# Kernel optimization log

Measured on AMD Instinct MI355X. Metric: run time of the kernel, lower is better.

## Reference

```python
import jax, jax.numpy as jnp
import numpy as np

N = 50000          # nodes
E = 1600000        # edges
F_IN = 128         # node_features
H = 256            # hidden_dim
A = 16             # action_dim
G = 64             # num graphs in batch


def _sage_conv(x, src, dst, Wl, bl, Wr, num_nodes):
    # PyG SAGEConv (aggr='mean'): out = lin_l(mean_{j in N(i)} x_j) + lin_r(x_i)
    msgs = x[src]                                              # [E, F] gather
    agg = jax.ops.segment_sum(msgs, dst, num_segments=num_nodes)
    cnt = jax.ops.segment_sum(jnp.ones((src.shape[0], 1), x.dtype), dst,
                              num_segments=num_nodes)
    mean = agg / jnp.maximum(cnt, 1.0)                         # [N, F]
    return mean @ Wl + bl + x @ Wr


def setup_inputs() -> dict:
    key = jax.random.key(0)
    ks = jax.random.split(key, 16)
    s = lambda k, sh: jax.random.normal(k, sh, dtype=jnp.float32) * (1.0 / np.sqrt(sh[0]))
    inp = {
        "x": jax.random.normal(ks[0], (N, F_IN), dtype=jnp.float32),
        "edge_index": jax.random.randint(ks[1], (2, E), 0, N, dtype=jnp.int32),
        "batch": jnp.sort(jax.random.randint(ks[2], (N,), 0, G, dtype=jnp.int32)),
        # SAGEConv 1
        "Wl1": s(ks[3], (F_IN, H)), "bl1": jnp.zeros((H,), jnp.float32), "Wr1": s(ks[4], (F_IN, H)),
        # SAGEConv 2
        "Wl2": s(ks[5], (H, H)), "bl2": jnp.zeros((H,), jnp.float32), "Wr2": s(ks[6], (H, H)),
        # actor MLP
        "Wa1": s(ks[7], (H, H)), "ba1": jnp.zeros((H,), jnp.float32),
        "Wa2": s(ks[8], (H, A)), "ba2": jnp.zeros((A,), jnp.float32),
        # critic MLP
        "Wc1": s(ks[9], (H, H)), "bc1": jnp.zeros((H,), jnp.float32),
        "Wc2": s(ks[10], (H, 1)), "bc2": jnp.zeros((1,), jnp.float32),
    }
    return inp


def reference(x, edge_index, batch, Wl1, bl1, Wr1, Wl2, bl2, Wr2,
              Wa1, ba1, Wa2, ba2, Wc1, bc1, Wc2, bc2):
    src, dst = edge_index[0], edge_index[1]
    h = jax.nn.relu(_sage_conv(x, src, dst, Wl1, bl1, Wr1, N))
    h = jax.nn.relu(_sage_conv(h, src, dst, Wl2, bl2, Wr2, N))
    # global_mean_pool over graph ids
    pooled = jax.ops.segment_sum(h, batch, num_segments=G)
    gcnt = jax.ops.segment_sum(jnp.ones((N, 1), h.dtype), batch, num_segments=G)
    g = pooled / jnp.maximum(gcnt, 1.0)                        # [G, H]
    mu = jax.nn.relu(g @ Wa1 + ba1) @ Wa2 + ba2                # [G, A]
    value = jax.nn.relu(g @ Wc1 + bc1) @ Wc2 + bc2             # [G, 1]
    return mu, value
```

## Files before the change

kernel.cpp:

```cpp
#include <hip/hip_runtime.h>
#include <hip/hip_bf16.h>
#include <hip/hip_fp8.h>

#define NN 50000
#define NE 1600000
#define FIN 128
#define HH 256
#define GG 64
#define AA 16
#define NRANGE 4
#define RSZ (NN / NRANGE)
#define CAP 128
#define NFB ((NE / 4 + 255) / 256 * NRANGE)

typedef __attribute__((ext_vector_type(8))) short short8;
typedef __attribute__((ext_vector_type(4))) float f32x4;
typedef __attribute__((ext_vector_type(4))) int   i32x4;
typedef __attribute__((ext_vector_type(4))) uint  u32x4;

static __device__ __forceinline__ ushort f2b(float f) {
    union { __hip_bfloat16 h; ushort u; } v; v.h = __float2bfloat16(f); return v.u;
}
static __device__ __forceinline__ float b2f_lo(uint a) {
    union { float f; uint u; } v; v.u = a << 16; return v.f;
}
template<int SEL>
static __device__ __forceinline__ float f8tof(uint u) {
#if __has_builtin(__builtin_amdgcn_cvt_f32_fp8)
    return __builtin_amdgcn_cvt_f32_fp8(u, SEL);
#else
    union { unsigned char c; __hip_fp8_e4m3 f; } v;
    v.c = (u >> (SEL * 8)) & 0xFF;
    return (float)v.f;
#endif
}
static __device__ __forceinline__ unsigned char ftof8(float f) {
    __hip_fp8_e4m3 v(f);
    return *reinterpret_cast<unsigned char*>(&v);
}

__global__ void k_prep(const int* __restrict__ src, const int* __restrict__ dst,
                       int* __restrict__ cnt, ushort* __restrict__ csr16,
                       const float* __restrict__ x, ushort* __restrict__ xb,
                       unsigned char* __restrict__ xf8,
                       const float* __restrict__ Wl1, const float* __restrict__ Wr1,
                       ushort* __restrict__ Wt1,
                       const float* __restrict__ Wl2, const float* __restrict__ Wr2,
                       ushort* __restrict__ Wt2) {
    int b = blockIdx.x, t = threadIdx.x;
    if (b < NFB) {
        int range = b & (NRANGE - 1);
        int i = (b / NRANGE) * 256 + t;
        if (i >= NE / 4) return;
        i32x4 d = __builtin_nontemporal_load(reinterpret_cast<const i32x4*>(dst) + i);
        i32x4 s = __builtin_nontemporal_load(reinterpret_cast<const i32x4*>(src) + i);
        int lo = range * RSZ, hi = lo + RSZ;
        if (d.x >= lo && d.x < hi) {
            int sl = atomicAdd(&cnt[d.x], 1);
            if (sl < CAP) csr16[(size_t)d.x * CAP + sl] = (ushort)s.x;
        }
        if (d.y >= lo && d.y < hi) {
            int sl = atomicAdd(&cnt[d.y], 1);
            if (sl < CAP) csr16[(size_t)d.y * CAP + sl] = (ushort)s.y;
        }
        if (d.z >= lo && d.z < hi) {
            int sl = atomicAdd(&cnt[d.z], 1);
            if (sl < CAP) csr16[(size_t)d.z * CAP + sl] = (ushort)s.z;
        }
        if (d.w >= lo && d.w < hi) {
            int sl = atomicAdd(&cnt[d.w], 1);
            if (sl < CAP) csr16[(size_t)d.w * CAP + sl] = (ushort)s.w;
        }
    } else if (b < NFB + 6250) {
        int i = (b - NFB) * 256 + t;
        float4 v = reinterpret_cast<const float4*>(x)[i];
        ushort4 o; o.x = f2b(v.x); o.y = f2b(v.y); o.z = f2b(v.z); o.w = f2b(v.w);
        reinterpret_cast<ushort4*>(xb)[i] = o;
        uchar4 p; p.x = ftof8(v.x); p.y = ftof8(v.y); p.z = ftof8(v.z); p.w = ftof8(v.w);
        reinterpret_cast<uchar4*>(xf8)[i] = p;
    } else if (b < NFB + 6506) {
        int i = (b - NFB - 6250) * 256 + t;
        int n = i / 256, k = i % 256;
        float v = (k < 128) ? Wl1[k * HH + n] : Wr1[(k - 128) * HH + n];
        Wt1[i] = f2b(v);
    } else {
        int i = (b - NFB - 6506) * 256 + t;
        int n = i / 512, k = i % 512;
        float v = (k < 256) ? Wl2[k * HH + n] : Wr2[(k - 256) * HH + n];
        Wt2[i] = f2b(v);
    }
}

template<int C>
__global__ void __launch_bounds__(256) k_gatherf8(
        const int* __restrict__ cnt, const ushort* __restrict__ csr16,
        const unsigned char* __restrict__ feat, ushort* __restrict__ agg) {
    constexpr int V = C / 64;
    int wid = threadIdx.x >> 6, lane = threadIdx.x & 63;
    int node = blockIdx.x * 4 + wid;
    if (node >= NN) return;
    int deg = cnt[node]; if (deg > CAP) deg = CAP;
    const ushort* row = csr16 + (size_t)node * CAP;
    const unsigned char* fp = feat + lane * V;
    float acc[V];
#pragma unroll
    for (int i = 0; i < V; i++) acc[i] = 0.0f;

    int t = 0;
    for (; t + 3 < deg; t += 4) {
        int s0 = __builtin_nontemporal_load(row + t);
        int s1 = __builtin_nontemporal_load(row + t + 1);
        int s2 = __builtin_nontemporal_load(row + t + 2);
        int s3 = __builtin_nontemporal_load(row + t + 3);
        if constexpr (V == 2) {
            uint u0 = *(const ushort*)(fp + (size_t)s0 * C);
            uint u1 = *(const ushort*)(fp + (size_t)s1 * C);
            uint u2 = *(const ushort*)(fp + (size_t)s2 * C);
            uint u3 = *(const ushort*)(fp + (size_t)s3 * C);
            acc[0] += (f8tof<0>(u0) + f8tof<0>(u1)) + (f8tof<0>(u2) + f8tof<0>(u3));
            acc[1] += (f8tof<1>(u0) + f8tof<1>(u1)) + (f8tof<1>(u2) + f8tof<1>(u3));
        } else {
            uint u0 = *(const uint*)(fp + (size_t)s0 * C);
            uint u1 = *(const uint*)(fp + (size_t)s1 * C);
            uint u2 = *(const uint*)(fp + (size_t)s2 * C);
            uint u3 = *(const uint*)(fp + (size_t)s3 * C);
            acc[0] += (f8tof<0>(u0) + f8tof<0>(u1)) + (f8tof<0>(u2) + f8tof<0>(u3));
            acc[1] += (f8tof<1>(u0) + f8tof<1>(u1)) + (f8tof<1>(u2) + f8tof<1>(u3));
            acc[2] += (f8tof<2>(u0) + f8tof<2>(u1)) + (f8tof<2>(u2) + f8tof<2>(u3));
            acc[3] += (f8tof<3>(u0) + f8tof<3>(u1)) + (f8tof<3>(u2) + f8tof<3>(u3));
        }
    }
    for (; t < deg; ++t) {
        int s0 = __builtin_nontemporal_load(row + t);
        if constexpr (V == 2) {
            uint u0 = *(const ushort*)(fp + (size_t)s0 * C);
            acc[0] += f8tof<0>(u0); acc[1] += f8tof<1>(u0);
        } else {
            uint u0 = *(const uint*)(fp + (size_t)s0 * C);
            acc[0] += f8tof<0>(u0); acc[1] += f8tof<1>(u0);
            acc[2] += f8tof<2>(u0); acc[3] += f8tof<3>(u0);
        }
    }

    float r = __builtin_amdgcn_rcpf(deg > 1 ? (float)deg : 1.0f);
    if constexpr (V == 2) {
        uint o = (uint)f2b(acc[0] * r) | ((uint)f2b(acc[1] * r) << 16);
        *(uint*)(agg + (size_t)node * C + lane * 2) = o;
    } else {
        uint2 o;
        o.x = (uint)f2b(acc[0] * r) | ((uint)f2b(acc[1] * r) << 16);
        o.y = (uint)f2b(acc[2] * r) | ((uint)f2b(acc[3] * r) << 16);
        *(uint2*)(agg + (size_t)node * C + lane * 4) = o;
    }
}

template<int K>
__global__ void __launch_bounds__(256) k_sage_mfma(
        const ushort* __restrict__ agg, const ushort* __restrict__ xin,
        const ushort* __restrict__ Wt, const float* __restrict__ bias,
        ushort* __restrict__ outb, unsigned char* __restrict__ out8) {
    constexpr int KH = K / 2;
    constexpr int LDP = 40;
    __shared__ ushort As[128 * LDP];
    __shared__ ushort Bs[256 * LDP];

    const int tid  = threadIdx.x;
    const int lane = tid & 63;
    const int w    = tid >> 6;
    const int base = blockIdx.x * 128;
    const int r    = lane & 15;
    const int kh   = lane >> 4;
    const int wcol = w * 64;

    f32x4 acc[8][4];
#pragma unroll
    for (int m = 0; m < 8; m++)
#pragma unroll
        for (int n = 0; n < 4; n++) acc[m][n] = (f32x4){0.f, 0.f, 0.f, 0.f};

    const int frowA = tid >> 1;
    const int fqA   = tid & 1;
    const int frowB = tid >> 2;
    const int fqB   = tid & 3;
    int fnode = base + frowA; if (fnode >= NN) fnode = 0;

    for (int k0 = 0; k0 < K; k0 += 32) {
        __syncthreads();
        {
            const ushort* srcp = (k0 < KH)
                ? agg + (size_t)fnode * KH + k0 + fqA * 16
                : xin + (size_t)fnode * KH + (k0 - KH) + fqA * 16;
            u32x4 a0 = *(const u32x4*)srcp;
            u32x4 a1 = *(const u32x4*)(srcp + 8);
            *(u32x4*)(&As[frowA * LDP + fqA * 16])     = a0;
            *(u32x4*)(&As[frowA * LDP + fqA * 16 + 8]) = a1;
        }
#pragma unroll
        for (int s = 0; s < 4; s++) {
            int c = frowB + s * 64;
            *(u32x4*)(&Bs[c * LDP + fqB * 8]) =
                *(const u32x4*)(Wt + (size_t)c * K + k0 + fqB * 8);
        }
        __syncthreads();

        short8 av[8], bv[4];
#pragma unroll
        for (int m = 0; m < 8; m++)
            av[m] = *(const short8*)(&As[(m * 16 + r) * LDP + kh * 8]);
#pragma unroll
        for (int n = 0; n < 4; n++)
            bv[n] = *(const short8*)(&Bs[(wcol + n * 16 + r) * LDP + kh * 8]);
#pragma unroll
        for (int m = 0; m < 8; m++)
#pragma unroll
            for (int n = 0; n < 4; n++)
                acc[m][n] = __builtin_amdgcn_mfma_f32_16x16x32_bf16(
                    av[m], bv[n], acc[m][n], 0, 0, 0);
    }

    float bj[4];
#pragma unroll
    for (int n = 0; n < 4; n++) bj[n] = bias[wcol + n * 16 + r];

#pragma unroll
    for (int m = 0; m < 8; m++) {
        int rowbase = base + m * 16 + (lane >> 4) * 4;
#pragma unroll
        for (int reg = 0; reg < 4; reg++) {
            int nd = rowbase + reg;
            if (nd < NN) {
#pragma unroll
                for (int n = 0; n < 4; n++) {
                    float v = acc[m][n][reg] + bj[n];
                    v = v > 0.0f ? v : 0.0f;
                    outb[(size_t)nd * HH + wcol + n * 16 + r] = f2b(v);
                    if (out8) out8[(size_t)nd * HH + wcol + n * 16 + r] = ftof8(v);
                }
            }
        }
    }
}

__global__ void k_pool(const ushort* __restrict__ h, const int* __restrict__ batch,
                       float* __restrict__ gpool) {
    __shared__ int sb[32];
    int j = threadIdx.x;
    int base = blockIdx.x * 32;
    int n = NN - base; if (n > 32) n = 32;
    if (j < n) sb[j] = batch[base + j];
    __syncthreads();
    float acc = 0.0f;
    int cur = sb[0];
    for (int t = 0; t < n; t++) {
        int g = sb[t];
        if (g != cur) {
            atomicAdd(&gpool[cur * HH + j], acc);
            acc = 0.0f;
            cur = g;
        }
        acc += b2f_lo((uint)h[(size_t)(base + t) * HH + j]);
    }
    atomicAdd(&gpool[cur * HH + j], acc);
}

__global__ void k_head(const float* __restrict__ gpool, const int* __restrict__ batch,
                       const float* __restrict__ Wa1, const float* __restrict__ ba1,
                       const float* __restrict__ Wa2, const float* __restrict__ ba2,
                       const float* __restrict__ Wc1, const float* __restrict__ bc1,
                       const float* __restrict__ Wc2, const float* __restrict__ bc2,
                       float* __restrict__ outp) {
    __shared__ float gv[HH], ha[HH], hc[HH];
    __shared__ float cs;
    int g = blockIdx.x, j = threadIdx.x;
    if (j == 0) {
        int lo = 0, hi = NN;
        while (lo < hi) { int m = (lo + hi) >> 1; if (batch[m] < g) lo = m + 1; else hi = m; }
        int a = lo; lo = 0; hi = NN;
        while (lo < hi) { int m = (lo + hi) >> 1; if (batch[m] < g + 1) lo = m + 1; else hi = m; }
        cs = (float)(lo - a);
    }
    __syncthreads();
    float c = cs > 1.0f ? cs : 1.0f;
    gv[j] = gpool[g * HH + j] / c;
    __syncthreads();
    float a_acc = ba1[j], c_acc = bc1[j];
#pragma unroll 2
    for (int k = 0; k < HH; k += 4) {
        float4 g4 = *reinterpret_cast<const float4*>(&gv[k]);
        const float* WA = Wa1 + k * HH + j;
        const float* WC = Wc1 + k * HH + j;
        a_acc += g4.x * WA[0] + g4.y * WA[HH] + g4.z * WA[2 * HH] + g4.w * WA[3 * HH];
        c_acc += g4.x * WC[0] + g4.y * WC[HH] + g4.z * WC[2 * HH] + g4.w * WC[3 * HH];
    }
    ha[j] = a_acc > 0.0f ? a_acc : 0.0f;
    hc[j] = c_acc > 0.0f ? c_acc : 0.0f;
    __syncthreads();
    if (j < AA) {
        float m = ba2[j];
        for (int k = 0; k < HH; k++) m += ha[k] * Wa2[k * AA + j];
        outp[g * AA + j] = m;
    } else if (j == AA) {
        float v = bc2[0];
        for (int k = 0; k < HH; k++) v += hc[k] * Wc2[k];
        outp[GG * AA + g] = v;
    }
}

extern "C" void kernel_launch(void* const* d_in, const int* in_sizes, int n_in,
                              void* d_out, int out_size, void* d_ws, size_t ws_size,
                              hipStream_t stream) {
    const float* x     = (const float*)d_in[0];
    const int*   ei    = (const int*)d_in[1];
    const int*   batch = (const int*)d_in[2];
    const float* Wl1 = (const float*)d_in[3];
    const float* bl1 = (const float*)d_in[4];
    const float* Wr1 = (const float*)d_in[5];
    const float* Wl2 = (const float*)d_in[6];
    const float* bl2 = (const float*)d_in[7];
    const float* Wr2 = (const float*)d_in[8];
    const float* Wa1 = (const float*)d_in[9];
    const float* ba1 = (const float*)d_in[10];
    const float* Wa2 = (const float*)d_in[11];
    const float* ba2 = (const float*)d_in[12];
    const float* Wc1 = (const float*)d_in[13];
    const float* bc1 = (const float*)d_in[14];
    const float* Wc2 = (const float*)d_in[15];
    const float* bc2 = (const float*)d_in[16];
    float* out = (float*)d_out;

    const int* srcv = ei;
    const int* dstv = ei + NE;

    char* ws = (char*)d_ws;
    int*    cnt      = (int*)(ws + 0);
    float*  gpool    = (float*)(ws + 200192);
    ushort* csr16    = (ushort*)(ws + 265728);
    ushort* xb       = (ushort*)(ws + 13065728);
    ushort* agg1b    = (ushort*)(ws + 25865728);
    ushort* h1b      = (ushort*)(ws + 38665728);
    ushort* agg2b    = (ushort*)(ws + 64265728);
    ushort* Wt1      = (ushort*)(ws + 89865728);
    ushort* Wt2      = (ushort*)(ws + 89996800);
    unsigned char* xf8  = (unsigned char*)(ws + 90258944);
    unsigned char* h1f8 = (unsigned char*)(ws + 96658944);

    (void)hipMemsetAsync(ws, 0, 265728, stream);

    k_prep<<<NFB + 7018, 256, 0, stream>>>(srcv, dstv, cnt, csr16,
                                           x, xb, xf8, Wl1, Wr1, Wt1, Wl2, Wr2, Wt2);

    k_gatherf8<FIN><<<(NN + 3) / 4, 256, 0, stream>>>(cnt, csr16, xf8, agg1b);
    k_sage_mfma<2 * FIN><<<(NN + 127) / 128, 256, 0, stream>>>(agg1b, xb, Wt1, bl1, h1b, h1f8);

    k_gatherf8<HH><<<(NN + 3) / 4, 256, 0, stream>>>(cnt, csr16, h1f8, agg2b);
    k_sage_mfma<2 * HH><<<(NN + 127) / 128, 256, 0, stream>>>(agg2b, h1b, Wt2, bl2, agg2b, nullptr);

    k_pool<<<(NN + 31) / 32, 256, 0, stream>>>(agg2b, batch, gpool);
    k_head<<<GG, 256, 0, stream>>>(gpool, batch, Wa1, ba1, Wa2, ba2, Wc1, bc1,
                                   Wc2, bc2, out);
}
```

Baseline: 358.4 us.

## Fuse neighbor-mean gather into SAGE MFMA GEMM via shared-memory aggregate tile

Each SAGE layer's gather kernel and GEMM kernel become one kernel. A block of 64 nodes first builds its fp8 neighbor-mean rows in shared memory, then feeds them straight into the MFMA loop, loading only the self-feature half from global memory. This drops the bf16 aggregate write and read-back through HBM and one launch per layer. In exchange the GEMM tile shrinks from 128 to 64 rows, so weights are reloaded twice as often, and the gather phase may limit occupancy and latency hiding because of the larger LDS footprint.

```diff
diff --git a/kernel.cpp b/kernel.cpp
--- a/kernel.cpp
+++ b/kernel.cpp
@@ -91,127 +91,129 @@
     }
 }
 
-template<int C>
-__global__ void __launch_bounds__(256) k_gatherf8(
+template<int KH>
+__global__ void __launch_bounds__(256) k_gather_sage(
         const int* __restrict__ cnt, const ushort* __restrict__ csr16,
-        const unsigned char* __restrict__ feat, ushort* __restrict__ agg) {
-    constexpr int V = C / 64;
-    int wid = threadIdx.x >> 6, lane = threadIdx.x & 63;
-    int node = blockIdx.x * 4 + wid;
-    if (node >= NN) return;
-    int deg = cnt[node]; if (deg > CAP) deg = CAP;
-    const ushort* row = csr16 + (size_t)node * CAP;
-    const unsigned char* fp = feat + lane * V;
-    float acc[V];
-#pragma unroll
-    for (int i = 0; i < V; i++) acc[i] = 0.0f;
-
-    int t = 0;
-    for (; t + 3 < deg; t += 4) {
-        int s0 = __builtin_nontemporal_load(row + t);
-        int s1 = __builtin_nontemporal_load(row + t + 1);
-        int s2 = __builtin_nontemporal_load(row + t + 2);
-        int s3 = __builtin_nontemporal_load(row + t + 3);
-        if constexpr (V == 2) {
-            uint u0 = *(const ushort*)(fp + (size_t)s0 * C);
-            uint u1 = *(const ushort*)(fp + (size_t)s1 * C);
-            uint u2 = *(const ushort*)(fp + (size_t)s2 * C);
-            uint u3 = *(const ushort*)(fp + (size_t)s3 * C);
-            acc[0] += (f8tof<0>(u0) + f8tof<0>(u1)) + (f8tof<0>(u2) + f8tof<0>(u3));
-            acc[1] += (f8tof<1>(u0) + f8tof<1>(u1)) + (f8tof<1>(u2) + f8tof<1>(u3));
-        } else {
-            uint u0 = *(const uint*)(fp + (size_t)s0 * C);
-            uint u1 = *(const uint*)(fp + (size_t)s1 * C);
-            uint u2 = *(const uint*)(fp + (size_t)s2 * C);
-            uint u3 = *(const uint*)(fp + (size_t)s3 * C);
-            acc[0] += (f8tof<0>(u0) + f8tof<0>(u1)) + (f8tof<0>(u2) + f8tof<0>(u3));
-            acc[1] += (f8tof<1>(u0) + f8tof<1>(u1)) + (f8tof<1>(u2) + f8tof<1>(u3));
-            acc[2] += (f8tof<2>(u0) + f8tof<2>(u1)) + (f8tof<2>(u2) + f8tof<2>(u3));
-            acc[3] += (f8tof<3>(u0) + f8tof<3>(u1)) + (f8tof<3>(u2) + f8tof<3>(u3));
-        }
-    }
-    for (; t < deg; ++t) {
-        int s0 = __builtin_nontemporal_load(row + t);
-        if constexpr (V == 2) {
-            uint u0 = *(const ushort*)(fp + (size_t)s0 * C);
-            acc[0] += f8tof<0>(u0); acc[1] += f8tof<1>(u0);
-        } else {
-            uint u0 = *(const uint*)(fp + (size_t)s0 * C);
-            acc[0] += f8tof<0>(u0); acc[1] += f8tof<1>(u0);
-            acc[2] += f8tof<2>(u0); acc[3] += f8tof<3>(u0);
-        }
-    }
-
-    float r = __builtin_amdgcn_rcpf(deg > 1 ? (float)deg : 1.0f);
-    if constexpr (V == 2) {
-        uint o = (uint)f2b(acc[0] * r) | ((uint)f2b(acc[1] * r) << 16);
-        *(uint*)(agg + (size_t)node * C + lane * 2) = o;
-    } else {
-        uint2 o;
-        o.x = (uint)f2b(acc[0] * r) | ((uint)f2b(acc[1] * r) << 16);
-        o.y = (uint)f2b(acc[2] * r) | ((uint)f2b(acc[3] * r) << 16);
-        *(uint2*)(agg + (size_t)node * C + lane * 4) = o;
-    }
-}
-
-template<int K>
-__global__ void __launch_bounds__(256) k_sage_mfma(
-        const ushort* __restrict__ agg, const ushort* __restrict__ xin,
+        const unsigned char* __restrict__ feat8, const ushort* __restrict__ xin,
         const ushort* __restrict__ Wt, const float* __restrict__ bias,
         ushort* __restrict__ outb, unsigned char* __restrict__ out8) {
-    constexpr int KH = K / 2;
+    constexpr int K   = 2 * KH;
+    constexpr int V   = KH / 64;
+    constexpr int AGP = KH + 8;
     constexpr int LDP = 40;
-    __shared__ ushort As[128 * LDP];
+    __shared__ ushort agg_t[64 * AGP];
+    __shared__ ushort As[64 * LDP];
     __shared__ ushort Bs[256 * LDP];
 
     const int tid  = threadIdx.x;
     const int lane = tid & 63;
     const int w    = tid >> 6;
-    const int base = blockIdx.x * 128;
+    const int base = blockIdx.x * 64;
     const int r    = lane & 15;
     const int kh   = lane >> 4;
     const int wcol = w * 64;
 
-    f32x4 acc[8][4];
-#pragma unroll
-    for (int m = 0; m < 8; m++)
+    {
+        const unsigned char* fp = feat8 + lane * V;
+        for (int i = 0; i < 16; ++i) {
+            int nl = w * 16 + i;
+            int node = base + nl;
+            float acc[V];
+#pragma unroll
+            for (int q = 0; q < V; q++) acc[q] = 0.0f;
+            int deg = 0;
+            if (node < NN) {
+                deg = cnt[node]; if (deg > CAP) deg = CAP;
+                const ushort* row = csr16 + (size_t)node * CAP;
+                int t = 0;
+                for (; t + 3 < deg; t += 4) {
+                    int s0 = __builtin_nontemporal_load(row + t);
+                    int s1 = __builtin_nontemporal_load(row + t + 1);
+                    int s2 = __builtin_nontemporal_load(row + t + 2);
+                    int s3 = __builtin_nontemporal_load(row + t + 3);
+                    if constexpr (V == 2) {
+                        uint u0 = *(const ushort*)(fp + (size_t)s0 * KH);
+                        uint u1 = *(const ushort*)(fp + (size_t)s1 * KH);
+                        uint u2 = *(const ushort*)(fp + (size_t)s2 * KH);
+                        uint u3 = *(const ushort*)(fp + (size_t)s3 * KH);
+                        acc[0] += (f8tof<0>(u0) + f8tof<0>(u1)) + (f8tof<0>(u2) + f8tof<0>(u3));
+                        acc[1] += (f8tof<1>(u0) + f8tof<1>(u1)) + (f8tof<1>(u2) + f8tof<1>(u3));
+                    } else {
+                        uint u0 = *(const uint*)(fp + (size_t)s0 * KH);
+                        uint u1 = *(const uint*)(fp + (size_t)s1 * KH);
+                        uint u2 = *(const uint*)(fp + (size_t)s2 * KH);
+                        uint u3 = *(const uint*)(fp + (size_t)s3 * KH);
+                        acc[0] += (f8tof<0>(u0) + f8tof<0>(u1)) + (f8tof<0>(u2) + f8tof<0>(u3));
+                        acc[1] += (f8tof<1>(u0) + f8tof<1>(u1)) + (f8tof<1>(u2) + f8tof<1>(u3));
+                        acc[2] += (f8tof<2>(u0) + f8tof<2>(u1)) + (f8tof<2>(u2) + f8tof<2>(u3));
+                        acc[3] += (f8tof<3>(u0) + f8tof<3>(u1)) + (f8tof<3>(u2) + f8tof<3>(u3));
+                    }
+                }
+                for (; t < deg; ++t) {
+                    int s0 = __builtin_nontemporal_load(row + t);
+                    if constexpr (V == 2) {
+                        uint u0 = *(const ushort*)(fp + (size_t)s0 * KH);
+                        acc[0] += f8tof<0>(u0); acc[1] += f8tof<1>(u0);
+                    } else {
+                        uint u0 = *(const uint*)(fp + (size_t)s0 * KH);
+                        acc[0] += f8tof<0>(u0); acc[1] += f8tof<1>(u0);
+                        acc[2] += f8tof<2>(u0); acc[3] += f8tof<3>(u0);
+                    }
+                }
+            }
+            float rr = __builtin_amdgcn_rcpf(deg > 1 ? (float)deg : 1.0f);
+            if constexpr (V == 2) {
+                uint o = (uint)f2b(acc[0] * rr) | ((uint)f2b(acc[1] * rr) << 16);
+                *(uint*)(&agg_t[nl * AGP + lane * 2]) = o;
+            } else {
+                uint2 o;
+                o.x = (uint)f2b(acc[0] * rr) | ((uint)f2b(acc[1] * rr) << 16);
+                o.y = (uint)f2b(acc[2] * rr) | ((uint)f2b(acc[3] * rr) << 16);
+                *(uint2*)(&agg_t[nl * AGP + lane * 4]) = o;
+            }
+        }
+    }
+    __syncthreads();
+
+    f32x4 acc[4][4];
+#pragma unroll
+    for (int m = 0; m < 4; m++)
 #pragma unroll
         for (int n = 0; n < 4; n++) acc[m][n] = (f32x4){0.f, 0.f, 0.f, 0.f};
 
-    const int frowA = tid >> 1;
-    const int fqA   = tid & 1;
-    const int frowB = tid >> 2;
-    const int fqB   = tid & 3;
-    int fnode = base + frowA; if (fnode >= NN) fnode = 0;
+    const int frow = tid >> 2;
+    const int fq   = tid & 3;
+    int fnode = base + frow; if (fnode >= NN) fnode = 0;
 
     for (int k0 = 0; k0 < K; k0 += 32) {
         __syncthreads();
-        {
-            const ushort* srcp = (k0 < KH)
-                ? agg + (size_t)fnode * KH + k0 + fqA * 16
-                : xin + (size_t)fnode * KH + (k0 - KH) + fqA * 16;
-            u32x4 a0 = *(const u32x4*)srcp;
-            u32x4 a1 = *(const u32x4*)(srcp + 8);
-            *(u32x4*)(&As[frowA * LDP + fqA * 16])     = a0;
-            *(u32x4*)(&As[frowA * LDP + fqA * 16 + 8]) = a1;
+        if (k0 >= KH) {
+            *(u32x4*)(&As[frow * LDP + fq * 8]) =
+                *(const u32x4*)(xin + (size_t)fnode * KH + (k0 - KH) + fq * 8);
         }
 #pragma unroll
         for (int s = 0; s < 4; s++) {
-            int c = frowB + s * 64;
-            *(u32x4*)(&Bs[c * LDP + fqB * 8]) =
-                *(const u32x4*)(Wt + (size_t)c * K + k0 + fqB * 8);
+            int c = frow + s * 64;
+            *(u32x4*)(&Bs[c * LDP + fq * 8]) =
+                *(const u32x4*)(Wt + (size_t)c * K + k0 + fq * 8);
         }
         __syncthreads();
 
-        short8 av[8], bv[4];
-#pragma unroll
-        for (int m = 0; m < 8; m++)
-            av[m] = *(const short8*)(&As[(m * 16 + r) * LDP + kh * 8]);
+        short8 av[4], bv[4];
+        if (k0 < KH) {
+#pragma unroll
+            for (int m = 0; m < 4; m++)
+                av[m] = *(const short8*)(&agg_t[(m * 16 + r) * AGP + k0 + kh * 8]);
+        } else {
+#pragma unroll
+            for (int m = 0; m < 4; m++)
+                av[m] = *(const short8*)(&As[(m * 16 + r) * LDP + kh * 8]);
+        }
 #pragma unroll
         for (int n = 0; n < 4; n++)
             bv[n] = *(const short8*)(&Bs[(wcol + n * 16 + r) * LDP + kh * 8]);
 #pragma unroll
-        for (int m = 0; m < 8; m++)
+        for (int m = 0; m < 4; m++)
 #pragma unroll
             for (int n = 0; n < 4; n++)
                 acc[m][n] = __builtin_amdgcn_mfma_f32_16x16x32_bf16(
@@ -223,7 +225,7 @@
     for (int n = 0; n < 4; n++) bj[n] = bias[wcol + n * 16 + r];
 
 #pragma unroll
-    for (int m = 0; m < 8; m++) {
+    for (int m = 0; m < 4; m++) {
         int rowbase = base + m * 16 + (lane >> 4) * 4;
 #pragma unroll
         for (int reg = 0; reg < 4; reg++) {
@@ -336,26 +338,25 @@
     float*  gpool    = (float*)(ws + 200192);
     ushort* csr16    = (ushort*)(ws + 265728);
     ushort* xb       = (ushort*)(ws + 13065728);
-    ushort* agg1b    = (ushort*)(ws + 25865728);
-    ushort* h1b      = (ushort*)(ws + 38665728);
-    ushort* agg2b    = (ushort*)(ws + 64265728);
-    ushort* Wt1      = (ushort*)(ws + 89865728);
-    ushort* Wt2      = (ushort*)(ws + 89996800);
-    unsigned char* xf8  = (unsigned char*)(ws + 90258944);
-    unsigned char* h1f8 = (unsigned char*)(ws + 96658944);
+    ushort* h1b      = (ushort*)(ws + 25865728);
+    ushort* h2b      = (ushort*)(ws + 51465728);
+    ushort* Wt1      = (ushort*)(ws + 77065728);
+    ushort* Wt2      = (ushort*)(ws + 77196800);
+    unsigned char* xf8  = (unsigned char*)(ws + 77458944);
+    unsigned char* h1f8 = (unsigned char*)(ws + 83858944);
 
     (void)hipMemsetAsync(ws, 0, 265728, stream);
 
     k_prep<<<NFB + 7018, 256, 0, stream>>>(srcv, dstv, cnt, csr16,
                                            x, xb, xf8, Wl1, Wr1, Wt1, Wl2, Wr2, Wt2);
 
-    k_gatherf8<FIN><<<(NN + 3) / 4, 256, 0, stream>>>(cnt, csr16, xf8, agg1b);
-    k_sage_mfma<2 * FIN><<<(NN + 127) / 128, 256, 0, stream>>>(agg1b, xb, Wt1, bl1, h1b, h1f8);
-
-    k_gatherf8<HH><<<(NN + 3) / 4, 256, 0, stream>>>(cnt, csr16, h1f8, agg2b);
-    k_sage_mfma<2 * HH><<<(NN + 127) / 128, 256, 0, stream>>>(agg2b, h1b, Wt2, bl2, agg2b, nullptr);
-
-    k_pool<<<(NN + 31) / 32, 256, 0, stream>>>(agg2b, batch, gpool);
+    k_gather_sage<FIN><<<(NN + 63) / 64, 256, 0, stream>>>(
+        cnt, csr16, xf8, xb, Wt1, bl1, h1b, h1f8);
+
+    k_gather_sage<HH><<<(NN + 63) / 64, 256, 0, stream>>>(
+        cnt, csr16, h1f8, h1b, Wt2, bl2, h2b, nullptr);
+
+    k_pool<<<(NN + 31) / 32, 256, 0, stream>>>(h2b, batch, gpool);
     k_head<<<GG, 256, 0, stream>>>(gpool, batch, Wa1, ba1, Wa2, ba2, Wc1, bc1,
                                    Wc2, bc2, out);
 }
```

Result: slower. 612.3 us (+70.9%).
